# Optimization experiments

Hardware: AMD Instinct MI355X
Metric: run time of the kernel (lower is better)

Reference implementation:

```python
import jax, jax.numpy as jnp
import numpy as np

N = 10000
E = 640000
F = 128      # in_dim
H = 4        # heads
Dh = 32      # head_dim = ceil(128/4)
INNER = H * Dh   # 128 == out_dim -> W_out is Identity
OUT = 128
SCALE = 1.0 / np.sqrt(float(Dh))
LN_EPS = 1e-5


def setup_inputs() -> dict:
    key = jax.random.key(0)
    ks = jax.random.split(key, 8)
    s = 1.0 / np.sqrt(F)
    nodes = jax.random.normal(ks[0], (N, F), dtype=jnp.float32)
    edge_index = jax.random.randint(ks[1], (2, E), 0, N, dtype=jnp.int32)
    W_Q = jax.random.uniform(ks[2], (F, INNER), jnp.float32, -s, s)
    W_K = jax.random.uniform(ks[3], (F, INNER), jnp.float32, -s, s)
    W_V = jax.random.uniform(ks[4], (F, INNER), jnp.float32, -s, s)
    W_res = jax.random.uniform(ks[5], (F, OUT), jnp.float32, -s, s)
    b_res = jax.random.uniform(ks[6], (OUT,), jnp.float32, -s, s)
    gamma = jnp.ones((OUT,), jnp.float32)
    beta = jnp.zeros((OUT,), jnp.float32)
    return {"nodes": nodes, "W_Q": W_Q, "W_K": W_K, "W_V": W_V,
            "W_res": W_res, "b_res": b_res, "gamma": gamma, "beta": beta,
            "edge_index": edge_index}


def reference(nodes, W_Q, W_K, W_V, W_res, b_res, gamma, beta, edge_index):
    n = nodes.shape[0]
    src = edge_index[0]
    dst = edge_index[1]
    # node-level projections, split into heads: [N, H, Dh]
    Q = (nodes @ W_Q).reshape(n, H, Dh)
    K = (nodes @ W_K).reshape(n, H, Dh)
    V = (nodes @ W_V).reshape(n, H, Dh)
    # per-edge gathers: q from dst, k/v from src
    q = Q[dst]          # [E, H, Dh]
    k = K[src]
    v = V[src]
    score = jnp.sum(q * k, axis=-1) * SCALE      # [E, H]
    # segment softmax over dst
    mx = jax.ops.segment_max(score, dst, num_segments=n)   # [N, H]
    mx = jnp.where(jnp.isfinite(mx), mx, 0.0)               # guard empty segments
    ex = jnp.exp(score - mx[dst])                           # [E, H]
    sm = jax.ops.segment_sum(ex, dst, num_segments=n)       # [N, H]
    alpha = ex / (sm[dst] + 1e-12)                          # [E, H]
    # scatter-aggregate weighted values
    agg = jax.ops.segment_sum(alpha[:, :, None] * v, dst, num_segments=n)  # [N, H, Dh]
    H_cat = agg.reshape(n, INNER)                # W_out is Identity (inner == out)
    H_out = H_cat + nodes @ W_res + b_res        # residual projection
    # LayerNorm(out_dim)
    mu = jnp.mean(H_out, axis=-1, keepdims=True)
    var = jnp.mean(jnp.square(H_out - mu), axis=-1, keepdims=True)
    x_hat = (H_out - mu) * jax.lax.rsqrt(var + LN_EPS)
    return gamma * x_hat + beta
```

## Files before the change

### kernel.cpp

```cpp
#include <hip/hip_runtime.h>
#include <math.h>

#define FDIM 128
#define NP 64
#define NMAX 10240
static constexpr float SC2 = 0.17677669529663687f * 1.4426950408889634f;
static constexpr float LN_EPS = 1e-5f;

typedef __attribute__((ext_vector_type(8))) short bf16x8;
typedef __attribute__((ext_vector_type(4))) float f32x4;

__device__ __forceinline__ unsigned short f2bf(float f) {
    unsigned u = __float_as_uint(f);
    unsigned r = u + 0x7FFFu + ((u >> 16) & 1u);
    return (unsigned short)(r >> 16);
}

__global__ __launch_bounds__(256) void prep_kernel(
    const float* __restrict__ Wq, const float* __restrict__ Wk,
    const float* __restrict__ Wv, const float* __restrict__ Wr,
    unsigned short* __restrict__ Wt)
{
    const int tid = threadIdx.x;
    const int t = blockIdx.x;
    const int wiW = t >> 2, q = t & 3;
    const float* __restrict__ W = (wiW == 0) ? Wq : (wiW == 1) ? Wk : (wiW == 2) ? Wv : Wr;
    const int c = q * 32 + (tid >> 3);
    const int k0 = (tid & 7) * 16;
    unsigned short* dp = &Wt[(size_t)wiW * 16384 + c * 128 + k0];
    #pragma unroll
    for (int kk = 0; kk < 16; ++kk)
        dp[kk] = f2bf(W[(k0 + kk) * FDIM + c]);
}

__global__ __launch_bounds__(256) void gemm_hist_kernel(
    const float* __restrict__ nodes,
    const unsigned short* __restrict__ Wt,
    const float* __restrict__ br,
    unsigned short* __restrict__ Qu, unsigned short* __restrict__ KVu,
    float* __restrict__ Rb, int N,
    const int* __restrict__ dst, int* __restrict__ bh, int E, int C)
{
    __shared__ __align__(16) char smem[52224];
    const int tid = threadIdx.x;
    const int wi = blockIdx.y;

    if (wi == 0) {
        const int p = blockIdx.x;
        if (p >= NP) return;
        int* h = (int*)smem;
        for (int i = tid; i < N; i += 256) h[i] = 0;
        __syncthreads();
        const int lo = p * C;
        const int hi = min(lo + C, E);
        const int n = hi - lo;
        if (n > 0) {
            if (((lo | E) & 3) == 0) {
                const int4* d4 = (const int4*)(dst + lo);
                const int n4 = n >> 2;
                for (int i = tid; i < n4; i += 256) {
                    int4 d = d4[i];
                    atomicAdd(&h[d.x], 1); atomicAdd(&h[d.y], 1);
                    atomicAdd(&h[d.z], 1); atomicAdd(&h[d.w], 1);
                }
                for (int i = lo + (n4 << 2) + tid; i < hi; i += 256)
                    atomicAdd(&h[dst[i]], 1);
            } else {
                for (int i = lo + tid; i < hi; i += 256)
                    atomicAdd(&h[dst[i]], 1);
            }
        }
        __syncthreads();
        for (int i = tid; i < N; i += 256) bh[p * N + i] = h[i];
        return;
    }

    const int gw = wi - 1;
    const int row0 = blockIdx.x * 64;
    unsigned short (*As)[136] = (unsigned short(*)[136])smem;
    unsigned short (*Ws)[136] = (unsigned short(*)[136])(smem + 64 * 272);

    #pragma unroll
    for (int i = 0; i < 8; ++i) {
        const int idx = tid + i * 256;
        const int r = idx >> 5, c4 = idx & 31;
        const int gr = row0 + r;
        float4 v = make_float4(0.f, 0.f, 0.f, 0.f);
        if (gr < N) v = *reinterpret_cast<const float4*>(&nodes[(size_t)gr * FDIM + c4 * 4]);
        ushort4 o;
        o.x = f2bf(v.x); o.y = f2bf(v.y); o.z = f2bf(v.z); o.w = f2bf(v.w);
        *reinterpret_cast<ushort4*>(&As[r][c4 * 4]) = o;
    }
    const unsigned short* Wg = &Wt[(size_t)gw * 16384];
    #pragma unroll
    for (int i = 0; i < 8; ++i) {
        const int idx = tid + i * 256;
        const int r = idx >> 4, ch = idx & 15;
        const uint4 v = *reinterpret_cast<const uint4*>(&Wg[r * 128 + ch * 8]);
        *reinterpret_cast<uint4*>(&Ws[r][ch * 8]) = v;
    }
    __syncthreads();

    const int w = tid >> 6;
    const int l = tid & 63;
    const int lr = l & 15;
    const int lh = l >> 4;

    f32x4 acc[8];
    #pragma unroll
    for (int ct = 0; ct < 8; ++ct) acc[ct] = (f32x4){0.f, 0.f, 0.f, 0.f};

    #pragma unroll
    for (int kc = 0; kc < 4; ++kc) {
        const bf16x8 a = *reinterpret_cast<const bf16x8*>(&As[w * 16 + lr][kc * 32 + lh * 8]);
        #pragma unroll
        for (int ct = 0; ct < 8; ++ct) {
            const bf16x8 bb = *reinterpret_cast<const bf16x8*>(&Ws[ct * 16 + lr][kc * 32 + lh * 8]);
            acc[ct] = __builtin_amdgcn_mfma_f32_16x16x32_bf16(a, bb, acc[ct], 0, 0, 0);
        }
    }

    const int rbase = row0 + w * 16 + lh * 4;
    #pragma unroll
    for (int ct = 0; ct < 8; ++ct) {
        const int col = ct * 16 + lr;
        float bc = 0.f;
        if (gw == 3) bc = br[col];
        #pragma unroll
        for (int r = 0; r < 4; ++r) {
            const int row = rbase + r;
            if (row >= N) continue;
            const float val = acc[ct][r];
            if (gw == 0)      Qu[(size_t)row * 128 + col] = f2bf(val);
            else if (gw == 1) KVu[(size_t)row * 256 + col] = f2bf(val);
            else if (gw == 2) KVu[(size_t)row * 256 + 128 + col] = f2bf(val);
            else              Rb[(size_t)row * 128 + col] = val + bc;
        }
    }
}

__global__ __launch_bounds__(256) void deg_kernel(
    const int* __restrict__ bh, int* __restrict__ deg, int N)
{
    const int d = blockIdx.x * 256 + threadIdx.x;
    if (d < N) {
        int s = 0;
        #pragma unroll
        for (int p = 0; p < NP; ++p) s += bh[p * N + d];
        deg[d] = s;
    }
}

__global__ __launch_bounds__(1024) void scan_kernel(
    const int* __restrict__ deg, int* __restrict__ rowptr, int N)
{
    __shared__ int tot[NMAX];
    __shared__ int wsum[16];
    const int tid = threadIdx.x;
    const int lane = tid & 63;
    const int wid = tid >> 6;

    for (int d = tid; d < N; d += 1024) tot[d] = deg[d];
    __syncthreads();

    const int CH = (N + 1023) / 1024;
    const int b = tid * CH;
    const int e = min(b + CH, N);
    int s = 0;
    for (int i = b; i < e; ++i) s += tot[i];

    int incl = s;
    #pragma unroll
    for (int off = 1; off < 64; off <<= 1) {
        int t = __shfl_up(incl, off);
        if (lane >= off) incl += t;
    }
    if (lane == 63) wsum[wid] = incl;
    __syncthreads();
    if (wid == 0) {
        int v = (lane < 16) ? wsum[lane] : 0;
        #pragma unroll
        for (int off = 1; off < 16; off <<= 1) {
            int t = __shfl_up(v, off);
            if (lane >= off) v += t;
        }
        if (lane < 16) wsum[lane] = v;
    }
    __syncthreads();
    const int wbase = (wid > 0) ? wsum[wid - 1] : 0;
    int run = wbase + incl - s;
    for (int i = b; i < e; ++i) {
        const int t = tot[i];
        rowptr[i] = run;
        run += t;
    }
    if (tid == 1023) rowptr[N] = wsum[15];
}

__global__ __launch_bounds__(256) void base_kernel(
    int* __restrict__ bh, const int* __restrict__ rowptr, int N)
{
    const int d = blockIdx.x * 256 + threadIdx.x;
    if (d < N) {
        int c = rowptr[d];
        #pragma unroll
        for (int p = 0; p < NP; ++p) {
            const int cnt = bh[p * N + d];
            bh[p * N + d] = c;
            c += cnt;
        }
    }
}

__global__ __launch_bounds__(256) void scatter_kernel(
    const int* __restrict__ src, const int* __restrict__ dst,
    const int* __restrict__ base, int* __restrict__ ssrc,
    int N, int E, int C)
{
    __shared__ int cur[NMAX];
    const int p = blockIdx.x, tid = threadIdx.x;
    for (int d = tid; d < N; d += 256) cur[d] = base[p * N + d];
    __syncthreads();

    const int lo = p * C;
    const int hi = min(lo + C, E);
    const int n = hi - lo;
    if (n <= 0) return;

    if (((lo | E) & 3) == 0) {
        const int4* s4 = (const int4*)(src + lo);
        const int4* d4 = (const int4*)(dst + lo);
        const int n4 = n >> 2;
        for (int i = tid; i < n4; i += 256) {
            int4 s = s4[i];
            int4 d = d4[i];
            int p0 = atomicAdd(&cur[d.x], 1); ssrc[p0] = s.x;
            int p1 = atomicAdd(&cur[d.y], 1); ssrc[p1] = s.y;
            int p2 = atomicAdd(&cur[d.z], 1); ssrc[p2] = s.z;
            int p3 = atomicAdd(&cur[d.w], 1); ssrc[p3] = s.w;
        }
        for (int i = lo + (n4 << 2) + tid; i < hi; i += 256) {
            int pos = atomicAdd(&cur[dst[i]], 1); ssrc[pos] = src[i];
        }
    } else {
        for (int i = lo + tid; i < hi; i += 256) {
            int pos = atomicAdd(&cur[dst[i]], 1); ssrc[pos] = src[i];
        }
    }
}

__global__ __launch_bounds__(256) void agg_kernel(
    const unsigned short* __restrict__ Qu, const unsigned short* __restrict__ KVu,
    const float* __restrict__ Rb,
    const int* __restrict__ rowptr, const int* __restrict__ ssrc,
    const float* __restrict__ gamma, const float* __restrict__ beta,
    float* __restrict__ out, int N)
{
    const int wave = threadIdx.x >> 6;
    const int lane = threadIdx.x & 63;
    const int qtr = lane >> 4;
    const int lq = lane & 15;
    const int n = blockIdx.x * 16 + wave * 4 + qtr;
    if (n >= N) return;
    const int d0 = lq * 8;

    const uint4 qu = *reinterpret_cast<const uint4*>(&Qu[(size_t)n * 128 + d0]);
    const float qf0 = __uint_as_float(qu.x << 16), qf1 = __uint_as_float(qu.x & 0xFFFF0000u);
    const float qf2 = __uint_as_float(qu.y << 16), qf3 = __uint_as_float(qu.y & 0xFFFF0000u);
    const float qf4 = __uint_as_float(qu.z << 16), qf5 = __uint_as_float(qu.z & 0xFFFF0000u);
    const float qf6 = __uint_as_float(qu.w << 16), qf7 = __uint_as_float(qu.w & 0xFFFF0000u);

    const int beg = rowptr[n];
    const int end = rowptr[n + 1];

    float4 A0a = make_float4(0.f, 0.f, 0.f, 0.f), A0b = A0a;
    float4 A1a = A0a, A1b = A0a, A2a = A0a, A2b = A0a, A3a = A0a, A3b = A0a;
    float L0 = 0.f, L1 = 0.f, L2 = 0.f, L3 = 0.f;

#define GATHER(S, NK, NV)                                                     \
    {                                                                         \
        const unsigned short* bp = &KVu[(size_t)(S) * 256 + d0];              \
        NK = *reinterpret_cast<const uint4*>(bp);                             \
        NV = *reinterpret_cast<const uint4*>(bp + 128);                       \
    }
#define STEP(KU, VU, Aa, Ab, L)                                               \
    {                                                                         \
        const float k0 = __uint_as_float((KU).x << 16), k1 = __uint_as_float((KU).x & 0xFFFF0000u); \
        const float k2 = __uint_as_float((KU).y << 16), k3 = __uint_as_float((KU).y & 0xFFFF0000u); \
        const float k4 = __uint_as_float((KU).z << 16), k5 = __uint_as_float((KU).z & 0xFFFF0000u); \
        const float k6 = __uint_as_float((KU).w << 16), k7 = __uint_as_float((KU).w & 0xFFFF0000u); \
        float p = qf0 * k0 + qf1 * k1 + qf2 * k2 + qf3 * k3                   \
                + qf4 * k4 + qf5 * k5 + qf6 * k6 + qf7 * k7;                  \
        p += __shfl_xor(p, 1);                                                \
        p += __shfl_xor(p, 2);                                                \
        const float e1 = exp2f(p * SC2);                                      \
        const float v0 = __uint_as_float((VU).x << 16), v1 = __uint_as_float((VU).x & 0xFFFF0000u); \
        const float v2 = __uint_as_float((VU).y << 16), v3 = __uint_as_float((VU).y & 0xFFFF0000u); \
        const float v4 = __uint_as_float((VU).z << 16), v5 = __uint_as_float((VU).z & 0xFFFF0000u); \
        const float v6 = __uint_as_float((VU).w << 16), v7 = __uint_as_float((VU).w & 0xFFFF0000u); \
        Aa.x += e1 * v0; Aa.y += e1 * v1; Aa.z += e1 * v2; Aa.w += e1 * v3;   \
        Ab.x += e1 * v4; Ab.y += e1 * v5; Ab.z += e1 * v6; Ab.w += e1 * v7;   \
        L += e1;                                                              \
    }

    uint4 nk0, nv0, nk1, nv1, nk2, nv2, nk3, nv3;
    int j = beg;
    const int nb = (end - beg) >> 2;
    if (nb > 0) {
        int c0i = ssrc[j], c1i = ssrc[j + 1], c2i = ssrc[j + 2], c3i = ssrc[j + 3];
        GATHER(c0i, nk0, nv0); GATHER(c1i, nk1, nv1);
        GATHER(c2i, nk2, nv2); GATHER(c3i, nk3, nv3);
        int x0 = ssrc[j + 4], x1 = ssrc[j + 5], x2 = ssrc[j + 6], x3 = ssrc[j + 7];
        for (int bi = 1; bi < nb; ++bi) {
            const uint4 ck0 = nk0, cv0 = nv0, ck1 = nk1, cv1 = nv1;
            const uint4 ck2 = nk2, cv2 = nv2, ck3 = nk3, cv3 = nv3;
            c0i = x0; c1i = x1; c2i = x2; c3i = x3;
            const int nbase = j + (bi + 1) * 4;
            x0 = ssrc[nbase]; x1 = ssrc[nbase + 1];
            x2 = ssrc[nbase + 2]; x3 = ssrc[nbase + 3];
            GATHER(c0i, nk0, nv0); GATHER(c1i, nk1, nv1);
            GATHER(c2i, nk2, nv2); GATHER(c3i, nk3, nv3);
            STEP(ck0, cv0, A0a, A0b, L0);
            STEP(ck1, cv1, A1a, A1b, L1);
            STEP(ck2, cv2, A2a, A2b, L2);
            STEP(ck3, cv3, A3a, A3b, L3);
        }
        STEP(nk0, nv0, A0a, A0b, L0);
        STEP(nk1, nv1, A1a, A1b, L1);
        STEP(nk2, nv2, A2a, A2b, L2);
        STEP(nk3, nv3, A3a, A3b, L3);
        j = beg + nb * 4;
    }
    for (; j < end; ++j) {
        const int s0 = ssrc[j];
        uint4 k0u, v0u;
        GATHER(s0, k0u, v0u);
        STEP(k0u, v0u, A0a, A0b, L0);
    }
#undef GATHER
#undef STEP

    const float L = (L0 + L1) + (L2 + L3);
    const float inv = 1.f / (L + 1e-12f);
    const float4 ra = *reinterpret_cast<const float4*>(&Rb[(size_t)n * 128 + d0]);
    const float4 rb = *reinterpret_cast<const float4*>(&Rb[(size_t)n * 128 + d0 + 4]);
    float xa0 = ((A0a.x + A1a.x) + (A2a.x + A3a.x)) * inv + ra.x;
    float xa1 = ((A0a.y + A1a.y) + (A2a.y + A3a.y)) * inv + ra.y;
    float xa2 = ((A0a.z + A1a.z) + (A2a.z + A3a.z)) * inv + ra.z;
    float xa3 = ((A0a.w + A1a.w) + (A2a.w + A3a.w)) * inv + ra.w;
    float xb0 = ((A0b.x + A1b.x) + (A2b.x + A3b.x)) * inv + rb.x;
    float xb1 = ((A0b.y + A1b.y) + (A2b.y + A3b.y)) * inv + rb.y;
    float xb2 = ((A0b.z + A1b.z) + (A2b.z + A3b.z)) * inv + rb.z;
    float xb3 = ((A0b.w + A1b.w) + (A2b.w + A3b.w)) * inv + rb.w;

    float s1v = (xa0 + xa1 + xa2 + xa3) + (xb0 + xb1 + xb2 + xb3);
    float s2v = xa0 * xa0 + xa1 * xa1 + xa2 * xa2 + xa3 * xa3
              + xb0 * xb0 + xb1 * xb1 + xb2 * xb2 + xb3 * xb3;
    #pragma unroll
    for (int off = 8; off; off >>= 1) {
        s1v += __shfl_xor(s1v, off);
        s2v += __shfl_xor(s2v, off);
    }
    const float mu = s1v * (1.f / 128.f);
    float var = s2v * (1.f / 128.f) - mu * mu;
    var = fmaxf(var, 0.f);
    const float rs = rsqrtf(var + LN_EPS);

    const float4 ga = *reinterpret_cast<const float4*>(&gamma[d0]);
    const float4 gb = *reinterpret_cast<const float4*>(&gamma[d0 + 4]);
    const float4 ba = *reinterpret_cast<const float4*>(&beta[d0]);
    const float4 bb = *reinterpret_cast<const float4*>(&beta[d0 + 4]);
    float4 oa, ob;
    oa.x = ga.x * (xa0 - mu) * rs + ba.x;
    oa.y = ga.y * (xa1 - mu) * rs + ba.y;
    oa.z = ga.z * (xa2 - mu) * rs + ba.z;
    oa.w = ga.w * (xa3 - mu) * rs + ba.w;
    ob.x = gb.x * (xb0 - mu) * rs + bb.x;
    ob.y = gb.y * (xb1 - mu) * rs + bb.y;
    ob.z = gb.z * (xb2 - mu) * rs + bb.z;
    ob.w = gb.w * (xb3 - mu) * rs + bb.w;
    *reinterpret_cast<float4*>(&out[(size_t)n * 128 + d0]) = oa;
    *reinterpret_cast<float4*>(&out[(size_t)n * 128 + d0 + 4]) = ob;
}

extern "C" void kernel_launch(void* const* d_in, const int* in_sizes, int n_in,
                              void* d_out, int out_size, void* d_ws, size_t ws_size,
                              hipStream_t stream)
{
    const float* nodes = (const float*)d_in[0];
    const float* W_Q   = (const float*)d_in[1];
    const float* W_K   = (const float*)d_in[2];
    const float* W_V   = (const float*)d_in[3];
    const float* W_res = (const float*)d_in[4];
    const float* b_res = (const float*)d_in[5];
    const float* gamma = (const float*)d_in[6];
    const float* beta  = (const float*)d_in[7];
    const int*   eidx  = (const int*)d_in[8];

    const int N = in_sizes[0] / FDIM;
    const int E = in_sizes[8] / 2;
    const int* src = eidx;
    const int* dst = eidx + E;

    float* out = (float*)d_out;

    unsigned short* KVu = (unsigned short*)d_ws;
    unsigned short* Qu  = KVu + (size_t)N * 256;
    unsigned short* Wt  = Qu + (size_t)N * 128;
    float* Rb   = (float*)(Wt + 4 * 16384);
    int* bh     = (int*)(Rb + (size_t)N * 128);
    int* rowptr = bh + (size_t)NP * N;
    int* deg    = rowptr + (N + 1);
    int* ssrc   = deg + N;

    const int C = (((E + NP - 1) / NP) + 3) & ~3;
    const int nG = (N + 63) / 64;
    const int nB = (N + 255) / 256;

    prep_kernel<<<16, 256, 0, stream>>>(W_Q, W_K, W_V, W_res, Wt);

    dim3 ggrid(nG, 5);
    gemm_hist_kernel<<<ggrid, 256, 0, stream>>>(nodes, Wt, b_res,
                                                Qu, KVu, Rb, N, dst, bh, E, C);
    deg_kernel<<<nB, 256, 0, stream>>>(bh, deg, N);
    scan_kernel<<<1, 1024, 0, stream>>>(deg, rowptr, N);
    base_kernel<<<nB, 256, 0, stream>>>(bh, rowptr, N);
    scatter_kernel<<<NP, 256, 0, stream>>>(src, dst, bh, ssrc, N, E, C);
    agg_kernel<<<(N + 15) / 16, 256, 0, stream>>>(Qu, KVu, Rb, rowptr, ssrc,
                                                  gamma, beta, out, N);
}
```

Measured before the change: 95.28 us.

## Record per-edge histogram ranks to make CSR scatter atomic-free and wider

```diff
diff --git a/kernel.cpp b/kernel.cpp
--- a/kernel.cpp
+++ b/kernel.cpp
@@ -39,7 +39,8 @@
     const float* __restrict__ br,
     unsigned short* __restrict__ Qu, unsigned short* __restrict__ KVu,
     float* __restrict__ Rb, int N,
-    const int* __restrict__ dst, int* __restrict__ bh, int E, int C)
+    const int* __restrict__ dst, int* __restrict__ bh,
+    int* __restrict__ rank, int E, int C)
 {
     __shared__ __align__(16) char smem[52224];
     const int tid = threadIdx.x;
@@ -57,17 +58,22 @@
         if (n > 0) {
             if (((lo | E) & 3) == 0) {
                 const int4* d4 = (const int4*)(dst + lo);
+                int4* r4p = (int4*)(rank + lo);
                 const int n4 = n >> 2;
                 for (int i = tid; i < n4; i += 256) {
                     int4 d = d4[i];
-                    atomicAdd(&h[d.x], 1); atomicAdd(&h[d.y], 1);
-                    atomicAdd(&h[d.z], 1); atomicAdd(&h[d.w], 1);
+                    int4 r;
+                    r.x = atomicAdd(&h[d.x], 1);
+                    r.y = atomicAdd(&h[d.y], 1);
+                    r.z = atomicAdd(&h[d.z], 1);
+                    r.w = atomicAdd(&h[d.w], 1);
+                    r4p[i] = r;
                 }
                 for (int i = lo + (n4 << 2) + tid; i < hi; i += 256)
-                    atomicAdd(&h[dst[i]], 1);
+                    rank[i] = atomicAdd(&h[dst[i]], 1);
             } else {
                 for (int i = lo + tid; i < hi; i += 256)
-                    atomicAdd(&h[dst[i]], 1);
+                    rank[i] = atomicAdd(&h[dst[i]], 1);
             }
         }
         __syncthreads();
@@ -214,38 +220,37 @@
 
 __global__ __launch_bounds__(256) void scatter_kernel(
     const int* __restrict__ src, const int* __restrict__ dst,
-    const int* __restrict__ base, int* __restrict__ ssrc,
-    int N, int E, int C)
-{
-    __shared__ int cur[NMAX];
-    const int p = blockIdx.x, tid = threadIdx.x;
-    for (int d = tid; d < N; d += 256) cur[d] = base[p * N + d];
-    __syncthreads();
-
-    const int lo = p * C;
-    const int hi = min(lo + C, E);
+    const int* __restrict__ rank, const int* __restrict__ base,
+    int* __restrict__ ssrc, int N, int E, int C)
+{
+    const int p = blockIdx.x >> 3;
+    const int sub = blockIdx.x & 7;
+    const int CS = C >> 3;
+    const int lo = p * C + sub * CS;
+    const int hi = min(lo + CS, E);
     const int n = hi - lo;
     if (n <= 0) return;
+    const int* bp = &base[p * N];
 
     if (((lo | E) & 3) == 0) {
         const int4* s4 = (const int4*)(src + lo);
         const int4* d4 = (const int4*)(dst + lo);
+        const int4* r4 = (const int4*)(rank + lo);
         const int n4 = n >> 2;
-        for (int i = tid; i < n4; i += 256) {
-            int4 s = s4[i];
-            int4 d = d4[i];
-            int p0 = atomicAdd(&cur[d.x], 1); ssrc[p0] = s.x;
-            int p1 = atomicAdd(&cur[d.y], 1); ssrc[p1] = s.y;
-            int p2 = atomicAdd(&cur[d.z], 1); ssrc[p2] = s.z;
-            int p3 = atomicAdd(&cur[d.w], 1); ssrc[p3] = s.w;
-        }
-        for (int i = lo + (n4 << 2) + tid; i < hi; i += 256) {
-            int pos = atomicAdd(&cur[dst[i]], 1); ssrc[pos] = src[i];
-        }
+        for (int i = threadIdx.x; i < n4; i += 256) {
+            const int4 s = s4[i];
+            const int4 d = d4[i];
+            const int4 r = r4[i];
+            ssrc[bp[d.x] + r.x] = s.x;
+            ssrc[bp[d.y] + r.y] = s.y;
+            ssrc[bp[d.z] + r.z] = s.z;
+            ssrc[bp[d.w] + r.w] = s.w;
+        }
+        for (int i = lo + (n4 << 2) + threadIdx.x; i < hi; i += 256)
+            ssrc[bp[dst[i]] + rank[i]] = src[i];
     } else {
-        for (int i = lo + tid; i < hi; i += 256) {
-            int pos = atomicAdd(&cur[dst[i]], 1); ssrc[pos] = src[i];
-        }
+        for (int i = lo + threadIdx.x; i < hi; i += 256)
+            ssrc[bp[dst[i]] + rank[i]] = src[i];
     }
 }
 
@@ -411,9 +416,10 @@
     int* bh     = (int*)(Rb + (size_t)N * 128);
     int* rowptr = bh + (size_t)NP * N;
     int* deg    = rowptr + (N + 1);
-    int* ssrc   = deg + N;
-
-    const int C = (((E + NP - 1) / NP) + 3) & ~3;
+    int* rank   = deg + N;
+    int* ssrc   = rank + E;
+
+    const int C = (((E + NP - 1) / NP) + 31) & ~31;
     const int nG = (N + 63) / 64;
     const int nB = (N + 255) / 256;
 
@@ -421,11 +427,11 @@
 
     dim3 ggrid(nG, 5);
     gemm_hist_kernel<<<ggrid, 256, 0, stream>>>(nodes, Wt, b_res,
-                                                Qu, KVu, Rb, N, dst, bh, E, C);
+                                                Qu, KVu, Rb, N, dst, bh, rank, E, C);
     deg_kernel<<<nB, 256, 0, stream>>>(bh, deg, N);
     scan_kernel<<<1, 1024, 0, stream>>>(deg, rowptr, N);
     base_kernel<<<nB, 256, 0, stream>>>(bh, rowptr, N);
-    scatter_kernel<<<NP, 256, 0, stream>>>(src, dst, bh, ssrc, N, E, C);
+    scatter_kernel<<<NP * 8, 256, 0, stream>>>(src, dst, rank, bh, ssrc, N, E, C);
     agg_kernel<<<(N + 15) / 16, 256, 0, stream>>>(Qu, KVu, Rb, rowptr, ssrc,
                                                   gamma, beta, out, N);
 }
```

Result: faster. 88.52 us (-7.1%).
